# Optimization experiments

Hardware: AMD Instinct MI355X
Metric: run time of the kernel (lower is better)

## Reference

```python
import jax, jax.numpy as jnp
import numpy as np

B, C, W, H = 16, 512, 32, 32
CQ = C // 2
WSCALE = 0.05  # keep energy logits in a sane range for softmax


def setup_inputs() -> dict:
    key = jax.random.key(0)
    ks = jax.random.split(key, 6)
    return {
        "x": jax.random.normal(ks[0], (B, C, W, H), dtype=jnp.float32),
        "Wq": jax.random.normal(ks[1], (CQ, C), dtype=jnp.float32) * WSCALE,
        "bq": jnp.zeros((CQ,), dtype=jnp.float32),
        "Wk": jax.random.normal(ks[2], (CQ, C), dtype=jnp.float32) * WSCALE,
        "bk": jnp.zeros((CQ,), dtype=jnp.float32),
        "Wv": jax.random.normal(ks[3], (C, C), dtype=jnp.float32) * WSCALE,
        "bv": jnp.zeros((C,), dtype=jnp.float32),
        "Wa": jax.random.normal(ks[4], (1, C), dtype=jnp.float32) * WSCALE,
        "ba": jnp.zeros((1,), dtype=jnp.float32),
        "gamma": jax.random.normal(ks[5], (1,), dtype=jnp.float32) * 0.1,
    }


def reference(x, Wq, bq, Wk, bk, Wv, bv, Wa, ba, gamma):
    b, c, w, h = x.shape
    n = w * h
    xf = x.reshape(b, c, n)  # flatten spatial: B,C,N
    # 1x1 convs == per-position channel matmuls
    q = jnp.einsum('oc,bcn->bon', Wq, xf) + bq[None, :, None]  # B,C/2,N
    k = jnp.einsum('oc,bcn->bon', Wk, xf) + bk[None, :, None]  # B,C/2,N
    v = jnp.einsum('oc,bcn->bon', Wv, xf) + bv[None, :, None]  # B,C,N
    # energy[b,i,j] = <q[:, i], k[:, j]>  (unscaled, single head)
    energy = jnp.einsum('bci,bcj->bij', q, k)  # B,N,N
    attn = jax.nn.softmax(energy, axis=-1)
    # out[b,c,i] = sum_j v[b,c,j] * attn[b,i,j]
    out = jnp.einsum('bcj,bij->bci', v, attn).reshape(b, c, w, h)
    # agnostic gating: 1x1 conv C->1 + sigmoid, gate = 1 - sigmoid
    ag = jax.nn.sigmoid(jnp.einsum('oc,bchw->bohw', Wa, out) + ba[None, :, None, None])
    out_A = out * (1.0 - ag)
    out_final = gamma[0] * out + x
    return (out_final, out_A)
```

## Files before the change

### kernel.cpp

```cpp
#include <hip/hip_runtime.h>
#include <hip/hip_bf16.h>
#include <math.h>

#define B 16
#define C 512
#define CQ 256
#define N 1024

typedef short bf16x8 __attribute__((ext_vector_type(8)));
typedef _Float16 f16x8 __attribute__((ext_vector_type(8)));
typedef float f32x4 __attribute__((ext_vector_type(4)));
typedef unsigned short ushort;

__device__ __forceinline__ unsigned short f2bf(float f) {
    __hip_bfloat16 h = __float2bfloat16(f);
    return *(unsigned short*)&h;
}
__device__ __forceinline__ ushort f2h(float f) {
    _Float16 h = (_Float16)f;
    return *(ushort*)&h;
}
__device__ __forceinline__ float h2f(ushort u) {
    _Float16 h = *(_Float16*)&u;
    return (float)h;
}
__device__ __forceinline__ f16x8 as_h(bf16x8 v) {
    union { bf16x8 s; f16x8 h; } u; u.s = v; return u.h;
}

__device__ __forceinline__ void gload16(void* lds, const void* g) {
    __builtin_amdgcn_global_load_lds(
        (const __attribute__((address_space(1))) void*)g,
        (__attribute__((address_space(3))) void*)lds, 16, 0, 0);
}

__device__ __forceinline__ void barrier_lgkm() {
    asm volatile("s_waitcnt lgkmcnt(0)" ::: "memory");
    __builtin_amdgcn_s_barrier();
    __builtin_amdgcn_sched_barrier(0);
}

template<int OUT_MODE, int BIAS_MODE, int XSWZ, int DT>
__global__ __launch_bounds__(256) void gemm128s(
    const ushort* __restrict__ A, long long sA,
    const ushort* __restrict__ BT, long long sB,
    void* __restrict__ Ch, long long sC,
    const float* __restrict__ bias, int K, int Ncols)
{
    __shared__ __align__(16) ushort As[128 * 128];
    __shared__ __align__(16) ushort Bs[128 * 128];

    int bx, by, bz;
    if constexpr (XSWZ) {
        const int lin  = blockIdx.x + gridDim.x * (blockIdx.y + gridDim.y * blockIdx.z);
        const int xcd  = lin & 7;
        const int slot = lin >> 3;
        bz = xcd + 8 * (slot >> 5);
        const int wxy = slot & 31;
        bx = wxy % gridDim.x;
        by = wxy / gridDim.x;
    } else {
        bx = blockIdx.x; by = blockIdx.y; bz = blockIdx.z;
    }

    const int tid  = threadIdx.x;
    const int lane = tid & 63;
    const int w    = tid >> 6;
    const int wr   = (w >> 1) * 64;
    const int wc   = (w & 1) * 64;
    const int fr   = lane & 15;
    const int ko2  = (lane >> 4) * 16;

    const int brow = by * 128;
    const int bcol = bx * 128;
    const size_t K2 = (size_t)K * 2;

    const char* Ab = (const char*)(A  + (size_t)bz * sA + (size_t)brow * K);
    const char* Bb = (const char*)(BT + (size_t)bz * sB + (size_t)bcol * K);

    const int sr = tid >> 4;
    const int ss = (tid & 15) * 16;

    f32x4 acc[4][4] = {};

    for (int k0 = 0; k0 < K; k0 += 128) {
#pragma unroll
        for (int p = 0; p < 8; ++p) {
            const int row = p * 16 + sr;
            const size_t so = (size_t)row * K2 + (size_t)k0 * 2
                            + (size_t)(ss ^ ((row & 15) << 4));
            gload16((char*)As + p * 4096 + tid * 16, Ab + so);
            gload16((char*)Bs + p * 4096 + tid * 16, Bb + so);
        }
        __syncthreads();
#pragma unroll
        for (int k32 = 0; k32 < 4; ++k32) {
            const int kswz = (k32 * 64 + ko2) ^ (fr << 4);
            bf16x8 ah[4], bh[4];
#pragma unroll
            for (int m = 0; m < 4; ++m)
                ah[m] = *(const bf16x8*)((const char*)As + (wr + m * 16 + fr) * 256 + kswz);
#pragma unroll
            for (int n = 0; n < 4; ++n)
                bh[n] = *(const bf16x8*)((const char*)Bs + (wc + n * 16 + fr) * 256 + kswz);
            if constexpr (DT == 1) {
#pragma unroll
                for (int m = 0; m < 4; ++m)
#pragma unroll
                    for (int n = 0; n < 4; ++n)
                        acc[m][n] = __builtin_amdgcn_mfma_f32_16x16x32_f16(
                            as_h(ah[m]), as_h(bh[n]), acc[m][n], 0, 0, 0);
            } else {
#pragma unroll
                for (int m = 0; m < 4; ++m)
#pragma unroll
                    for (int n = 0; n < 4; ++n)
                        acc[m][n] = __builtin_amdgcn_mfma_f32_16x16x32_bf16(
                            ah[m], bh[n], acc[m][n], 0, 0, 0);
            }
        }
        __syncthreads();
    }

    const int crow = brow + wr + (lane >> 4) * 4;
    const int ccol = bcol + wc + fr;
    const size_t cbase = (size_t)bz * sC;
#pragma unroll
    for (int m = 0; m < 4; ++m) {
#pragma unroll
        for (int n = 0; n < 4; ++n) {
            float cb = (BIAS_MODE == 2) ? bias[ccol + n * 16] : 0.f;
#pragma unroll
            for (int r = 0; r < 4; ++r) {
                int row = crow + m * 16 + r;
                int col = ccol + n * 16;
                float vv = acc[m][n][r];
                if (BIAS_MODE == 1) vv += bias[row];
                if (BIAS_MODE == 2) vv += cb;
                size_t idx = cbase + (size_t)row * Ncols + col;
                if (OUT_MODE == 0)      ((float*)Ch)[idx]  = vv;
                else if (OUT_MODE == 1) ((ushort*)Ch)[idx] = f2bf(vv);
                else                    ((ushort*)Ch)[idx] = f2h(vv);
            }
        }
    }
}

__global__ __launch_bounds__(512, 2) void fused_attn(
    const ushort* __restrict__ qk, const ushort* __restrict__ vmat,
    const float* __restrict__ Wa, const float* __restrict__ ba,
    const float* __restrict__ gamma, const float* __restrict__ x,
    float* __restrict__ dout)
{
    __shared__ __align__(16) char lds[149504];
    __shared__ float redbuf[2][2][4][32];
    __shared__ float redA[8][64];
    __shared__ float agL[64];

    const int tid  = threadIdx.x;
    const int lane = tid & 63;
    const int w    = tid >> 6;
    const int g    = w >> 2;
    const int wg4  = w & 3;
    const int fr   = lane & 15;
    const int il0  = (lane >> 4) * 4;
    const int ko2  = (lane >> 4) * 16;

    const int wgid = blockIdx.x + gridDim.x * blockIdx.y;
    const int nid  = (wgid & 7) * 32 + (wgid >> 3);
    const int b    = nid >> 4;
    const int i0   = (nid & 15) * 64;

    const char* qkB = (const char*)qk + (size_t)b * N * 1024;
    const char* vB  = (const char*)vmat + (size_t)b * C * N * 2;

    const int srow = tid >> 4;
    const int ssg  = (tid & 15) * 16;

    f16x8 a_h[2][2][4];
#pragma unroll
    for (int ks0 = 0; ks0 < 2; ++ks0)
#pragma unroll
        for (int m = 0; m < 2; ++m) {
            const char* qr = qkB + (size_t)(i0 + g * 32 + m * 16 + fr) * 1024
                           + ks0 * 256 + (lane >> 4) * 16;
#pragma unroll
            for (int k32 = 0; k32 < 4; ++k32)
                a_h[ks0][m][k32] = *(const f16x8*)(qr + k32 * 64);
        }

    auto stageK = [&](int s) {
        const int jt_  = s & 7;
        const int ks0_ = s >> 3;
        char* dst = lds + (s & 3) * 32768;
#pragma unroll
        for (int p = 0; p < 4; ++p) {
            const int row = p * 32 + srow;
            const size_t so = (size_t)(jt_ * 128 + row) * 1024 + 512
                            + (size_t)(ks0_ * 256)
                            + (size_t)(ssg ^ ((row & 15) << 4));
            gload16(dst + p * 8192 + tid * 16, qkB + so);
        }
    };

    f32x4 acc[16][2];
#pragma unroll
    for (int jt = 0; jt < 16; ++jt)
#pragma unroll
        for (int m = 0; m < 2; ++m)
            acc[jt][m] = (f32x4){0.f, 0.f, 0.f, 0.f};

    stageK(0);
    stageK(1);

#pragma unroll
    for (int s = 0; s < 16; ++s) {
        if (s + 2 < 16) stageK(s + 2);
        if (s < 14)       asm volatile("s_waitcnt vmcnt(8)" ::: "memory");
        else if (s == 14) asm volatile("s_waitcnt vmcnt(4)" ::: "memory");
        else              asm volatile("s_waitcnt vmcnt(0)" ::: "memory");
        __builtin_amdgcn_s_barrier();
        __builtin_amdgcn_sched_barrier(0);
        const char* kb = lds + (s & 3) * 32768;
        const int ks0 = s >> 3;
#pragma unroll
        for (int sub = 0; sub < 2; ++sub) {
            const int jrow = sub * 64 + wg4 * 16 + fr;
            const int rb   = jrow * 256;
            const int jidx = (s & 7) * 2 + sub;
#pragma unroll
            for (int k32 = 0; k32 < 4; ++k32) {
                const int kswz = (k32 * 64 + ko2) ^ (fr << 4);
                f16x8 b_h = *(const f16x8*)(kb + rb + kswz);
#pragma unroll
                for (int m = 0; m < 2; ++m)
                    acc[jidx][m] = __builtin_amdgcn_mfma_f32_16x16x32_f16(
                        a_h[ks0][m][k32], b_h, acc[jidx][m], 0, 0, 0);
            }
        }
    }

    auto stageV = [&](int j) {
        char* dst = lds + (j & 1) * 65536;
#pragma unroll
        for (int p = 0; p < 8; ++p) {
            const int ch = p * 512 + tid;
            const int row = ch >> 3;
            const int sg  = (ch & 7) * 16;
            const size_t so = (size_t)row * (N * 2) + (size_t)(j * 128)
                            + (size_t)(sg ^ ((row & 7) << 4));
            gload16(dst + ch * 16, vB + so);
        }
    };
    stageV(0);

    float mx[2][4];
#pragma unroll
    for (int m = 0; m < 2; ++m)
#pragma unroll
        for (int r = 0; r < 4; ++r) {
            float v = acc[0][m][r];
#pragma unroll
            for (int jt = 1; jt < 16; ++jt) v = fmaxf(v, acc[jt][m][r]);
            mx[m][r] = v;
        }
#pragma unroll
    for (int off = 1; off < 16; off <<= 1)
#pragma unroll
        for (int m = 0; m < 2; ++m)
#pragma unroll
            for (int r = 0; r < 4; ++r)
                mx[m][r] = fmaxf(mx[m][r], __shfl_xor(mx[m][r], off, 64));
    if (fr == 0) {
#pragma unroll
        for (int m = 0; m < 2; ++m)
#pragma unroll
            for (int r = 0; r < 4; ++r)
                redbuf[0][g][wg4][m * 16 + il0 + r] = mx[m][r];
    }
    barrier_lgkm();
#pragma unroll
    for (int m = 0; m < 2; ++m)
#pragma unroll
        for (int r = 0; r < 4; ++r) {
            const int row = m * 16 + il0 + r;
            mx[m][r] = fmaxf(fmaxf(redbuf[0][g][0][row], redbuf[0][g][1][row]),
                             fmaxf(redbuf[0][g][2][row], redbuf[0][g][3][row]));
        }

    float sm[2][4] = {};
#pragma unroll
    for (int jt = 0; jt < 16; ++jt)
#pragma unroll
        for (int m = 0; m < 2; ++m) {
            f32x4 e;
#pragma unroll
            for (int r = 0; r < 4; ++r) {
                e[r] = __expf(acc[jt][m][r] - mx[m][r]);
                sm[m][r] += e[r];
            }
            acc[jt][m] = e;
        }
#pragma unroll
    for (int off = 1; off < 16; off <<= 1)
#pragma unroll
        for (int m = 0; m < 2; ++m)
#pragma unroll
            for (int r = 0; r < 4; ++r)
                sm[m][r] += __shfl_xor(sm[m][r], off, 64);
    if (fr == 0) {
#pragma unroll
        for (int m = 0; m < 2; ++m)
#pragma unroll
            for (int r = 0; r < 4; ++r)
                redbuf[1][g][wg4][m * 16 + il0 + r] = sm[m][r];
    }
    barrier_lgkm();
#pragma unroll
    for (int m = 0; m < 2; ++m)
#pragma unroll
        for (int r = 0; r < 4; ++r) {
            const int row = m * 16 + il0 + r;
            float s = redbuf[1][g][0][row] + redbuf[1][g][1][row]
                    + redbuf[1][g][2][row] + redbuf[1][g][3][row];
            mx[m][r] = 1.f / s;
        }

    char* pPb = lds + 131072;
    f32x4 apv[4][4] = {};

#pragma unroll
    for (int jt = 0; jt < 16; ++jt) {
        ushort* pS = (ushort*)(pPb + (jt & 1) * 9216);
#pragma unroll
        for (int m = 0; m < 2; ++m) {
            const int lr = g * 32 + m * 16 + il0;
#pragma unroll
            for (int r = 0; r < 4; ++r)
                pS[(lr + r) * 72 + wg4 * 16 + fr] = f2h(acc[jt][m][r] * mx[m][r]);
        }
        asm volatile("s_waitcnt vmcnt(0) lgkmcnt(0)" ::: "memory");
        __builtin_amdgcn_s_barrier();
        __builtin_amdgcn_sched_barrier(0);
        if (jt + 1 < 16) stageV(jt + 1);
        const char* vb = lds + (jt & 1) * 65536;
#pragma unroll
        for (int k32 = 0; k32 < 2; ++k32) {
            f16x8 af[4], bf[4];
#pragma unroll
            for (int cf = 0; cf < 4; ++cf) {
                const int row = w * 64 + cf * 16 + fr;
                const int kb  = (k32 * 64 + ko2) ^ ((fr & 7) << 4);
                af[cf] = *(const f16x8*)(vb + row * 128 + kb);
            }
#pragma unroll
            for (int f = 0; f < 4; ++f)
                bf[f] = *(const f16x8*)((const char*)pS
                        + (f * 16 + fr) * 144 + k32 * 64 + ko2);
#pragma unroll
            for (int cf = 0; cf < 4; ++cf)
#pragma unroll
                for (int f = 0; f < 4; ++f)
                    apv[cf][f] = __builtin_amdgcn_mfma_f32_16x16x32_f16(
                        af[cf], bf[f], apv[cf][f], 0, 0, 0);
        }
    }

    float pg[4] = {0.f, 0.f, 0.f, 0.f};
#pragma unroll
    for (int cf = 0; cf < 4; ++cf)
#pragma unroll
        for (int r = 0; r < 4; ++r) {
            const float wv = Wa[w * 64 + cf * 16 + il0 + r];
#pragma unroll
            for (int f = 0; f < 4; ++f)
                pg[f] += wv * apv[cf][f][r];
        }
#pragma unroll
    for (int off = 16; off < 64; off <<= 1)
#pragma unroll
        for (int f = 0; f < 4; ++f)
            pg[f] += __shfl_xor(pg[f], off, 64);
    if (lane < 16) {
#pragma unroll
        for (int f = 0; f < 4; ++f)
            redA[w][f * 16 + fr] = pg[f];
    }
    barrier_lgkm();
    if (tid < 64) {
        float s = ba[0];
#pragma unroll
        for (int k = 0; k < 8; ++k) s += redA[k][tid];
        agL[tid] = 1.f / (1.f + __expf(-s));
    }

    const size_t BCN = (size_t)B * C * N;
    const float gmm = gamma[0];
    float* oS = (float*)lds;

#pragma unroll
    for (int h = 0; h < 2; ++h) {
#pragma unroll
        for (int cf = 0; cf < 4; ++cf) {
            const int crow = w * 64 + cf * 16 + il0;
#pragma unroll
            for (int f = 0; f < 2; ++f) {
                const int col = f * 16 + fr;
#pragma unroll
                for (int r = 0; r < 4; ++r)
                    oS[(crow + r) * 33 + col] = apv[cf][2 * h + f][r];
            }
        }
        barrier_lgkm();
#pragma unroll
        for (int p = 0; p < 8; ++p) {
            const int ch  = p * 512 + tid;
            const int row = ch >> 3;
            const int sg  = ch & 7;
            const int ib  = h * 32 + sg * 4;
            f32x4 o = *(const f32x4*)&oS[row * 33 + sg * 4];
            const size_t idx = ((size_t)b * C + row) * N + i0 + ib;
            f32x4 xv = *(const f32x4*)&x[idx];
            f32x4 of, oa;
#pragma unroll
            for (int q = 0; q < 4; ++q) {
                of[q] = gmm * o[q] + xv[q];
                oa[q] = o[q] * (1.f - agL[ib + q]);
            }
            *(f32x4*)&dout[idx]       = of;
            *(f32x4*)&dout[BCN + idx] = oa;
        }
        barrier_lgkm();
    }
}

__global__ void transpose_x_f16(const float* __restrict__ x,
                                ushort* __restrict__ xT) {
    __shared__ float t[32][33];
    int b  = blockIdx.z;
    int c0 = blockIdx.y * 32;
    int n0 = blockIdx.x * 32;
    int tid = threadIdx.x;
    int tx = tid & 31;
    int ty = tid >> 5;
#pragma unroll
    for (int r = 0; r < 4; ++r)
        t[ty + r * 8][tx] = x[(size_t)b * C * N + (size_t)(c0 + ty + r * 8) * N + n0 + tx];
    __syncthreads();
#pragma unroll
    for (int r = 0; r < 4; ++r) {
        float v = t[tx][ty + r * 8];
        size_t idx = (size_t)b * N * C + (size_t)(n0 + ty + r * 8) * C + c0 + tx;
        xT[idx] = f2h(v);
    }
}

__global__ void prep_weights(const float* __restrict__ Wq, const float* __restrict__ Wk,
                             const float* __restrict__ Wv,
                             const float* __restrict__ bq, const float* __restrict__ bk,
                             ushort* __restrict__ Wqk, ushort* __restrict__ Wv16,
                             float* __restrict__ bqk) {
    int i = blockIdx.x * 256 + threadIdx.x;
    if (i < CQ * C) {
        Wqk[i]          = f2h(Wq[i]);
        Wqk[CQ * C + i] = f2h(Wk[i]);
    }
    if (i < C * C) Wv16[i] = f2h(Wv[i]);
    if (i < 512) bqk[i] = (i < CQ) ? bq[i] : bk[i - CQ];
}

extern "C" void kernel_launch(void* const* d_in, const int* in_sizes, int n_in,
                              void* d_out, int out_size, void* d_ws, size_t ws_size,
                              hipStream_t stream) {
    const float* x     = (const float*)d_in[0];
    const float* Wq    = (const float*)d_in[1];
    const float* bq    = (const float*)d_in[2];
    const float* Wk    = (const float*)d_in[3];
    const float* bk    = (const float*)d_in[4];
    const float* Wv    = (const float*)d_in[5];
    const float* bv    = (const float*)d_in[6];
    const float* Wa    = (const float*)d_in[7];
    const float* ba    = (const float*)d_in[8];
    const float* gamma = (const float*)d_in[9];
    float* out = (float*)d_out;

    const size_t MB = 1048576;
    char* ws = (char*)d_ws;
    ushort* v_     = (ushort*)(ws);
    ushort* qkT    = (ushort*)(ws + 16 * MB);
    ushort* Wqk    = (ushort*)(ws + 48 * MB);
    ushort* Wv16   = (ushort*)(ws + 48 * MB + 524288);
    float*  bqk    = (float*)(ws + 49 * MB);
    ushort* xT     = (ushort*)(ws + 80 * MB);
    const size_t need = 96 * MB;
    if (ws_size < need) return;

    dim3 blk(256);
    transpose_x_f16<<<dim3(N / 32, C / 32, B), blk, 0, stream>>>(x, xT);
    prep_weights<<<dim3(C * C / 256), blk, 0, stream>>>(
        Wq, Wk, Wv, bq, bk, Wqk, Wv16, bqk);

    gemm128s<3, 2, 1, 1><<<dim3(4, 8, B), blk, 0, stream>>>(
        xT, (long long)N * C, Wqk, 0,
        qkT, (long long)N * 512, bqk, C, 512);
    gemm128s<3, 1, 1, 1><<<dim3(8, 4, B), blk, 0, stream>>>(
        Wv16, 0, xT, (long long)N * C,
        v_, (long long)C * N, bv, C, N);
    fused_attn<<<dim3(16, 16), dim3(512), 0, stream>>>(
        qkT, v_, Wa, ba, gamma, x, out);
}
```

Baseline: 98.13 us.

## Double fused attention workgroup to 1024 threads, splitting key columns and channels across waves

The fused attention kernel now runs 16 waves per workgroup instead of 8. Each wave handles half the key columns in the QK phase and half the output channels in the PV phase, so per-wave accumulators and Q fragments shrink: the Q fragments are reloaded for the second K half instead of being held in registers. Softmax probabilities are pre-packed to fp16 pairs, and only half the waves write P for each tile. This lowers register pressure and adds latency-hiding waves. The cost is more barrier participants, wider cross-wave reductions, and one workgroup per CU given the large LDS footprint.

```diff
diff --git a/kernel.cpp b/kernel.cpp
--- a/kernel.cpp
+++ b/kernel.cpp
@@ -146,22 +146,22 @@
     }
 }
 
-__global__ __launch_bounds__(512, 2) void fused_attn(
+__global__ __launch_bounds__(1024) void fused_attn(
     const ushort* __restrict__ qk, const ushort* __restrict__ vmat,
     const float* __restrict__ Wa, const float* __restrict__ ba,
     const float* __restrict__ gamma, const float* __restrict__ x,
     float* __restrict__ dout)
 {
     __shared__ __align__(16) char lds[149504];
-    __shared__ float redbuf[2][2][4][32];
-    __shared__ float redA[8][64];
+    __shared__ float redbuf[2][2][8][32];
+    __shared__ float redA[16][64];
     __shared__ float agL[64];
 
     const int tid  = threadIdx.x;
     const int lane = tid & 63;
     const int w    = tid >> 6;
-    const int g    = w >> 2;
-    const int wg4  = w & 3;
+    const int g    = w >> 3;
+    const int wg8  = w & 7;
     const int fr   = lane & 15;
     const int il0  = (lane >> 4) * 4;
     const int ko2  = (lane >> 4) * 16;
@@ -177,74 +177,78 @@
     const int srow = tid >> 4;
     const int ssg  = (tid & 15) * 16;
 
-    f16x8 a_h[2][2][4];
-#pragma unroll
-    for (int ks0 = 0; ks0 < 2; ++ks0)
-#pragma unroll
-        for (int m = 0; m < 2; ++m) {
-            const char* qr = qkB + (size_t)(i0 + g * 32 + m * 16 + fr) * 1024
-                           + ks0 * 256 + (lane >> 4) * 16;
-#pragma unroll
-            for (int k32 = 0; k32 < 4; ++k32)
-                a_h[ks0][m][k32] = *(const f16x8*)(qr + k32 * 64);
-        }
+    f16x8 a_h[2][4];
+#pragma unroll
+    for (int m = 0; m < 2; ++m) {
+        const char* qr = qkB + (size_t)(i0 + g * 32 + m * 16 + fr) * 1024
+                       + (lane >> 4) * 16;
+#pragma unroll
+        for (int k32 = 0; k32 < 4; ++k32)
+            a_h[m][k32] = *(const f16x8*)(qr + k32 * 64);
+    }
 
     auto stageK = [&](int s) {
         const int jt_  = s & 7;
         const int ks0_ = s >> 3;
         char* dst = lds + (s & 3) * 32768;
 #pragma unroll
-        for (int p = 0; p < 4; ++p) {
-            const int row = p * 32 + srow;
+        for (int p = 0; p < 2; ++p) {
+            const int row = p * 64 + srow;
             const size_t so = (size_t)(jt_ * 128 + row) * 1024 + 512
                             + (size_t)(ks0_ * 256)
                             + (size_t)(ssg ^ ((row & 15) << 4));
-            gload16(dst + p * 8192 + tid * 16, qkB + so);
+            gload16(dst + p * 16384 + tid * 16, qkB + so);
         }
     };
 
-    f32x4 acc[16][2];
-#pragma unroll
-    for (int jt = 0; jt < 16; ++jt)
+    f32x4 acc[8][2];
+#pragma unroll
+    for (int sl = 0; sl < 8; ++sl)
 #pragma unroll
         for (int m = 0; m < 2; ++m)
-            acc[jt][m] = (f32x4){0.f, 0.f, 0.f, 0.f};
+            acc[sl][m] = (f32x4){0.f, 0.f, 0.f, 0.f};
 
     stageK(0);
     stageK(1);
 
 #pragma unroll
     for (int s = 0; s < 16; ++s) {
+        if (s == 8) {
+#pragma unroll
+            for (int m = 0; m < 2; ++m) {
+                const char* qr = qkB + (size_t)(i0 + g * 32 + m * 16 + fr) * 1024
+                               + 256 + (lane >> 4) * 16;
+#pragma unroll
+                for (int k32 = 0; k32 < 4; ++k32)
+                    a_h[m][k32] = *(const f16x8*)(qr + k32 * 64);
+            }
+        }
         if (s + 2 < 16) stageK(s + 2);
-        if (s < 14)       asm volatile("s_waitcnt vmcnt(8)" ::: "memory");
-        else if (s == 14) asm volatile("s_waitcnt vmcnt(4)" ::: "memory");
+        if (s < 14)       asm volatile("s_waitcnt vmcnt(4)" ::: "memory");
+        else if (s == 14) asm volatile("s_waitcnt vmcnt(2)" ::: "memory");
         else              asm volatile("s_waitcnt vmcnt(0)" ::: "memory");
         __builtin_amdgcn_s_barrier();
         __builtin_amdgcn_sched_barrier(0);
         const char* kb = lds + (s & 3) * 32768;
-        const int ks0 = s >> 3;
-#pragma unroll
-        for (int sub = 0; sub < 2; ++sub) {
-            const int jrow = sub * 64 + wg4 * 16 + fr;
-            const int rb   = jrow * 256;
-            const int jidx = (s & 7) * 2 + sub;
-#pragma unroll
-            for (int k32 = 0; k32 < 4; ++k32) {
-                const int kswz = (k32 * 64 + ko2) ^ (fr << 4);
-                f16x8 b_h = *(const f16x8*)(kb + rb + kswz);
-#pragma unroll
-                for (int m = 0; m < 2; ++m)
-                    acc[jidx][m] = __builtin_amdgcn_mfma_f32_16x16x32_f16(
-                        a_h[ks0][m][k32], b_h, acc[jidx][m], 0, 0, 0);
-            }
+        const int sl   = s & 7;
+        const int jrow = wg8 * 16 + fr;
+        const int rb   = jrow * 256;
+#pragma unroll
+        for (int k32 = 0; k32 < 4; ++k32) {
+            const int kswz = (k32 * 64 + ko2) ^ (fr << 4);
+            f16x8 b_h = *(const f16x8*)(kb + rb + kswz);
+#pragma unroll
+            for (int m = 0; m < 2; ++m)
+                acc[sl][m] = __builtin_amdgcn_mfma_f32_16x16x32_f16(
+                    a_h[m][k32], b_h, acc[sl][m], 0, 0, 0);
         }
     }
 
     auto stageV = [&](int j) {
         char* dst = lds + (j & 1) * 65536;
 #pragma unroll
-        for (int p = 0; p < 8; ++p) {
-            const int ch = p * 512 + tid;
+        for (int p = 0; p < 4; ++p) {
+            const int ch = p * 1024 + tid;
             const int row = ch >> 3;
             const int sg  = (ch & 7) * 16;
             const size_t so = (size_t)row * (N * 2) + (size_t)(j * 128)
@@ -261,7 +265,7 @@
         for (int r = 0; r < 4; ++r) {
             float v = acc[0][m][r];
 #pragma unroll
-            for (int jt = 1; jt < 16; ++jt) v = fmaxf(v, acc[jt][m][r]);
+            for (int sl = 1; sl < 8; ++sl) v = fmaxf(v, acc[sl][m][r]);
             mx[m][r] = v;
         }
 #pragma unroll
@@ -276,7 +280,7 @@
         for (int m = 0; m < 2; ++m)
 #pragma unroll
             for (int r = 0; r < 4; ++r)
-                redbuf[0][g][wg4][m * 16 + il0 + r] = mx[m][r];
+                redbuf[0][g][wg8][m * 16 + il0 + r] = mx[m][r];
     }
     barrier_lgkm();
 #pragma unroll
@@ -284,22 +288,24 @@
 #pragma unroll
         for (int r = 0; r < 4; ++r) {
             const int row = m * 16 + il0 + r;
-            mx[m][r] = fmaxf(fmaxf(redbuf[0][g][0][row], redbuf[0][g][1][row]),
-                             fmaxf(redbuf[0][g][2][row], redbuf[0][g][3][row]));
+            float v = redbuf[0][g][0][row];
+#pragma unroll
+            for (int q = 1; q < 8; ++q) v = fmaxf(v, redbuf[0][g][q][row]);
+            mx[m][r] = v;
         }
 
     float sm[2][4] = {};
 #pragma unroll
-    for (int jt = 0; jt < 16; ++jt)
+    for (int sl = 0; sl < 8; ++sl)
 #pragma unroll
         for (int m = 0; m < 2; ++m) {
             f32x4 e;
 #pragma unroll
             for (int r = 0; r < 4; ++r) {
-                e[r] = __expf(acc[jt][m][r] - mx[m][r]);
+                e[r] = __expf(acc[sl][m][r] - mx[m][r]);
                 sm[m][r] += e[r];
             }
-            acc[jt][m] = e;
+            acc[sl][m] = e;
         }
 #pragma unroll
     for (int off = 1; off < 16; off <<= 1)
@@ -313,7 +319,7 @@
         for (int m = 0; m < 2; ++m)
 #pragma unroll
             for (int r = 0; r < 4; ++r)
-                redbuf[1][g][wg4][m * 16 + il0 + r] = sm[m][r];
+                redbuf[1][g][wg8][m * 16 + il0 + r] = sm[m][r];
     }
     barrier_lgkm();
 #pragma unroll
@@ -321,23 +327,42 @@
 #pragma unroll
         for (int r = 0; r < 4; ++r) {
             const int row = m * 16 + il0 + r;
-            float s = redbuf[1][g][0][row] + redbuf[1][g][1][row]
-                    + redbuf[1][g][2][row] + redbuf[1][g][3][row];
+            float s = redbuf[1][g][0][row];
+#pragma unroll
+            for (int q = 1; q < 8; ++q) s += redbuf[1][g][q][row];
             mx[m][r] = 1.f / s;
         }
 
+    unsigned hp[8][2][2];
+#pragma unroll
+    for (int sl = 0; sl < 8; ++sl)
+#pragma unroll
+        for (int m = 0; m < 2; ++m)
+#pragma unroll
+            for (int rp = 0; rp < 2; ++rp) {
+                const unsigned lo = f2h(acc[sl][m][rp * 2 + 0] * mx[m][rp * 2 + 0]);
+                const unsigned hi = f2h(acc[sl][m][rp * 2 + 1] * mx[m][rp * 2 + 1]);
+                hp[sl][m][rp] = lo | (hi << 16);
+            }
+
     char* pPb = lds + 131072;
-    f32x4 apv[4][4] = {};
+    f32x4 apv[2][4] = {};
 
 #pragma unroll
     for (int jt = 0; jt < 16; ++jt) {
         ushort* pS = (ushort*)(pPb + (jt & 1) * 9216);
-#pragma unroll
-        for (int m = 0; m < 2; ++m) {
-            const int lr = g * 32 + m * 16 + il0;
-#pragma unroll
-            for (int r = 0; r < 4; ++r)
-                pS[(lr + r) * 72 + wg4 * 16 + fr] = f2h(acc[jt][m][r] * mx[m][r]);
+        if ((wg8 >> 2) == (jt & 1)) {
+            const int colj = (wg8 & 3) * 16 + fr;
+#pragma unroll
+            for (int m = 0; m < 2; ++m) {
+                const int lr = g * 32 + m * 16 + il0;
+#pragma unroll
+                for (int rp = 0; rp < 2; ++rp) {
+                    const unsigned u = hp[jt >> 1][m][rp];
+                    pS[(lr + rp * 2 + 0) * 72 + colj] = (ushort)(u & 0xffffu);
+                    pS[(lr + rp * 2 + 1) * 72 + colj] = (ushort)(u >> 16);
+                }
+            }
         }
         asm volatile("s_waitcnt vmcnt(0) lgkmcnt(0)" ::: "memory");
         __builtin_amdgcn_s_barrier();
@@ -346,19 +371,19 @@
         const char* vb = lds + (jt & 1) * 65536;
 #pragma unroll
         for (int k32 = 0; k32 < 2; ++k32) {
-            f16x8 af[4], bf[4];
-#pragma unroll
-            for (int cf = 0; cf < 4; ++cf) {
-                const int row = w * 64 + cf * 16 + fr;
-                const int kb  = (k32 * 64 + ko2) ^ ((fr & 7) << 4);
-                af[cf] = *(const f16x8*)(vb + row * 128 + kb);
+            f16x8 af[2], bf[4];
+#pragma unroll
+            for (int cf = 0; cf < 2; ++cf) {
+                const int row = w * 32 + cf * 16 + fr;
+                const int kb2 = (k32 * 64 + ko2) ^ ((fr & 7) << 4);
+                af[cf] = *(const f16x8*)(vb + row * 128 + kb2);
             }
 #pragma unroll
             for (int f = 0; f < 4; ++f)
                 bf[f] = *(const f16x8*)((const char*)pS
                         + (f * 16 + fr) * 144 + k32 * 64 + ko2);
 #pragma unroll
-            for (int cf = 0; cf < 4; ++cf)
+            for (int cf = 0; cf < 2; ++cf)
 #pragma unroll
                 for (int f = 0; f < 4; ++f)
                     apv[cf][f] = __builtin_amdgcn_mfma_f32_16x16x32_f16(
@@ -368,10 +393,10 @@
 
     float pg[4] = {0.f, 0.f, 0.f, 0.f};
 #pragma unroll
-    for (int cf = 0; cf < 4; ++cf)
+    for (int cf = 0; cf < 2; ++cf)
 #pragma unroll
         for (int r = 0; r < 4; ++r) {
-            const float wv = Wa[w * 64 + cf * 16 + il0 + r];
+            const float wv = Wa[w * 32 + cf * 16 + il0 + r];
 #pragma unroll
             for (int f = 0; f < 4; ++f)
                 pg[f] += wv * apv[cf][f][r];
@@ -390,7 +415,7 @@
     if (tid < 64) {
         float s = ba[0];
 #pragma unroll
-        for (int k = 0; k < 8; ++k) s += redA[k][tid];
+        for (int k = 0; k < 16; ++k) s += redA[k][tid];
         agL[tid] = 1.f / (1.f + __expf(-s));
     }
 
@@ -401,8 +426,8 @@
 #pragma unroll
     for (int h = 0; h < 2; ++h) {
 #pragma unroll
-        for (int cf = 0; cf < 4; ++cf) {
-            const int crow = w * 64 + cf * 16 + il0;
+        for (int cf = 0; cf < 2; ++cf) {
+            const int crow = w * 32 + cf * 16 + il0;
 #pragma unroll
             for (int f = 0; f < 2; ++f) {
                 const int col = f * 16 + fr;
@@ -413,8 +438,8 @@
         }
         barrier_lgkm();
 #pragma unroll
-        for (int p = 0; p < 8; ++p) {
-            const int ch  = p * 512 + tid;
+        for (int p = 0; p < 4; ++p) {
+            const int ch  = p * 1024 + tid;
             const int row = ch >> 3;
             const int sg  = ch & 7;
             const int ib  = h * 32 + sg * 4;
@@ -506,6 +531,6 @@
     gemm128s<3, 1, 1, 1><<<dim3(8, 4, B), blk, 0, stream>>>(
         Wv16, 0, xT, (long long)N * C,
         v_, (long long)C * N, bv, C, N);
-    fused_attn<<<dim3(16, 16), dim3(512), 0, stream>>>(
+    fused_attn<<<dim3(16, 16), dim3(1024), 0, stream>>>(
         qkT, v_, Wa, ba, gamma, x, out);
 }
```

New measurement: 111.1 us. 1.13x slower.

## Read K and V operands directly from global memory instead of staging through LDS

Applied to the files above, without the earlier changes.

Drops the async global-to-LDS pipelines for the K tiles in the energy phase and the V tiles in the PV phase. MFMA operands are now loaded straight from global memory into registers, which removes the pipeline waits and some barriers. The LDS allocation shrinks to just the reduction and P buffers. The cost is that many waves re-read the same K/V rows from global or L2 with no prefetch overlap, so load latency is exposed directly to the MFMA loop.

```diff
diff --git a/kernel.cpp b/kernel.cpp
--- a/kernel.cpp
+++ b/kernel.cpp
@@ -19,10 +19,6 @@
 __device__ __forceinline__ ushort f2h(float f) {
     _Float16 h = (_Float16)f;
     return *(ushort*)&h;
-}
-__device__ __forceinline__ float h2f(ushort u) {
-    _Float16 h = *(_Float16*)&u;
-    return (float)h;
 }
 __device__ __forceinline__ f16x8 as_h(bf16x8 v) {
     union { bf16x8 s; f16x8 h; } u; u.s = v; return u.h;
@@ -152,7 +148,7 @@
     const float* __restrict__ gamma, const float* __restrict__ x,
     float* __restrict__ dout)
 {
-    __shared__ __align__(16) char lds[149504];
+    __shared__ __align__(16) char lds[86016];
     __shared__ float redbuf[2][2][4][32];
     __shared__ float redA[8][64];
     __shared__ float agL[64];
@@ -174,9 +170,6 @@
     const char* qkB = (const char*)qk + (size_t)b * N * 1024;
     const char* vB  = (const char*)vmat + (size_t)b * C * N * 2;
 
-    const int srow = tid >> 4;
-    const int ssg  = (tid & 15) * 16;
-
     f16x8 a_h[2][2][4];
 #pragma unroll
     for (int ks0 = 0; ks0 < 2; ++ks0)
@@ -189,20 +182,6 @@
                 a_h[ks0][m][k32] = *(const f16x8*)(qr + k32 * 64);
         }
 
-    auto stageK = [&](int s) {
-        const int jt_  = s & 7;
-        const int ks0_ = s >> 3;
-        char* dst = lds + (s & 3) * 32768;
-#pragma unroll
-        for (int p = 0; p < 4; ++p) {
-            const int row = p * 32 + srow;
-            const size_t so = (size_t)(jt_ * 128 + row) * 1024 + 512
-                            + (size_t)(ks0_ * 256)
-                            + (size_t)(ssg ^ ((row & 15) << 4));
-            gload16(dst + p * 8192 + tid * 16, qkB + so);
-        }
-    };
-
     f32x4 acc[16][2];
 #pragma unroll
     for (int jt = 0; jt < 16; ++jt)
@@ -210,28 +189,17 @@
         for (int m = 0; m < 2; ++m)
             acc[jt][m] = (f32x4){0.f, 0.f, 0.f, 0.f};
 
-    stageK(0);
-    stageK(1);
-
 #pragma unroll
     for (int s = 0; s < 16; ++s) {
-        if (s + 2 < 16) stageK(s + 2);
-        if (s < 14)       asm volatile("s_waitcnt vmcnt(8)" ::: "memory");
-        else if (s == 14) asm volatile("s_waitcnt vmcnt(4)" ::: "memory");
-        else              asm volatile("s_waitcnt vmcnt(0)" ::: "memory");
-        __builtin_amdgcn_s_barrier();
-        __builtin_amdgcn_sched_barrier(0);
-        const char* kb = lds + (s & 3) * 32768;
         const int ks0 = s >> 3;
 #pragma unroll
         for (int sub = 0; sub < 2; ++sub) {
-            const int jrow = sub * 64 + wg4 * 16 + fr;
-            const int rb   = jrow * 256;
+            const int jrow = (s & 7) * 128 + sub * 64 + wg4 * 16 + fr;
             const int jidx = (s & 7) * 2 + sub;
+            const char* kr = qkB + (size_t)jrow * 1024 + 512 + ks0 * 256;
 #pragma unroll
             for (int k32 = 0; k32 < 4; ++k32) {
-                const int kswz = (k32 * 64 + ko2) ^ (fr << 4);
-                f16x8 b_h = *(const f16x8*)(kb + rb + kswz);
+                f16x8 b_h = *(const f16x8*)(kr + k32 * 64 + ko2);
 #pragma unroll
                 for (int m = 0; m < 2; ++m)
                     acc[jidx][m] = __builtin_amdgcn_mfma_f32_16x16x32_f16(
@@ -239,20 +207,6 @@
             }
         }
     }
-
-    auto stageV = [&](int j) {
-        char* dst = lds + (j & 1) * 65536;
-#pragma unroll
-        for (int p = 0; p < 8; ++p) {
-            const int ch = p * 512 + tid;
-            const int row = ch >> 3;
-            const int sg  = (ch & 7) * 16;
-            const size_t so = (size_t)row * (N * 2) + (size_t)(j * 128)
-                            + (size_t)(sg ^ ((row & 7) << 4));
-            gload16(dst + ch * 16, vB + so);
-        }
-    };
-    stageV(0);
 
     float mx[2][4];
 #pragma unroll
@@ -326,7 +280,7 @@
             mx[m][r] = 1.f / s;
         }
 
-    char* pPb = lds + 131072;
+    char* pPb = lds + 67584;
     f32x4 apv[4][4] = {};
 
 #pragma unroll
@@ -339,19 +293,15 @@
             for (int r = 0; r < 4; ++r)
                 pS[(lr + r) * 72 + wg4 * 16 + fr] = f2h(acc[jt][m][r] * mx[m][r]);
         }
-        asm volatile("s_waitcnt vmcnt(0) lgkmcnt(0)" ::: "memory");
-        __builtin_amdgcn_s_barrier();
-        __builtin_amdgcn_sched_barrier(0);
-        if (jt + 1 < 16) stageV(jt + 1);
-        const char* vb = lds + (jt & 1) * 65536;
+        barrier_lgkm();
 #pragma unroll
         for (int k32 = 0; k32 < 2; ++k32) {
             f16x8 af[4], bf[4];
 #pragma unroll
             for (int cf = 0; cf < 4; ++cf) {
                 const int row = w * 64 + cf * 16 + fr;
-                const int kb  = (k32 * 64 + ko2) ^ ((fr & 7) << 4);
-                af[cf] = *(const f16x8*)(vb + row * 128 + kb);
+                af[cf] = *(const f16x8*)(vB + (size_t)row * 2048
+                                         + jt * 128 + k32 * 64 + ko2);
             }
 #pragma unroll
             for (int f = 0; f < 4; ++f)
```

Result: slower. 124.4 us (+26.8%).
